# Kernel tuning notes

Measured on AMD Instinct MI355X. Metric: run time of the kernel, lower is better.

## Reference

```python
import jax, jax.numpy as jnp
import numpy as np

C = 1.0
SQRT_C = 1.0
EPS = 1e-6

N_NODES = 50000
N_EDGES = 800000
IN_F = 128   # in_features (weight columns); x has IN_F+1 coords
OUT_F = 128  # out_features; output has OUT_F coords


def l_inner(x, y):
    # Lorentz inner product: -x0*y0 + sum_i xi*yi
    return jnp.sum(x[..., 1:] * y[..., 1:], axis=-1) - x[..., 0] * y[..., 0]


def arcosh(z):
    z = jnp.maximum(z, 1.0 + 1e-7)
    return jnp.log(z + jnp.sqrt(z * z - 1.0))


def log_map_zero(y):
    # log map at origin o=(sqrt(c),0,...,0); result is tangent with head 0
    dist = SQRT_C * arcosh(y[..., 0] / SQRT_C)                      # [N]
    tail = y[..., 1:]
    tail_norm = jnp.sqrt(jnp.maximum(jnp.sum(tail * tail, -1), EPS))
    scaled = (dist / tail_norm)[..., None] * tail
    return jnp.concatenate([jnp.zeros_like(y[..., :1]), scaled], -1)


def exp_map_zero(v):
    # v is a tangent vector at the origin with head component 0
    tail = v[..., 1:]
    n = jnp.sqrt(jnp.maximum(jnp.sum(tail * tail, -1, keepdims=True), EPS))
    n_cut = jnp.minimum(n, 50.0)
    new_tail = SQRT_C * jnp.sinh(n_cut / SQRT_C) * tail / n
    # project onto the hyperboloid: x0 = sqrt(c + ||tail||^2)
    head = jnp.sqrt(C + jnp.sum(new_tail * new_tail, -1, keepdims=True))
    return jnp.concatenate([head, new_tail], -1)


def matvec_regular(weight, x, bias):
    # LGCNLinear forward (eval mode: dropout is identity)
    x_tan = log_map_zero(x)                      # [N, IN_F+1], head = 0
    mx = x_tan[..., 1:] @ weight.T + bias        # [N, OUT_F-1]
    v = jnp.concatenate([x_tan[..., :1], mx], -1)  # head stays 0 (tangent-zero normalized)
    return exp_map_zero(v)                       # [N, OUT_F]


def lorentz_centroid(x, row, col, val):
    # sparse spmm aggregation + Lorentz centroid renormalization
    n = x.shape[0]
    msgs = val[:, None] * x[col]                               # [E, OUT_F] gather
    s = jax.ops.segment_sum(msgs, row, num_segments=n)         # [N, OUT_F] scatter-add
    inner = l_inner(s, s)                                      # [N]
    coef = SQRT_C / jnp.sqrt(jnp.maximum(jnp.abs(inner), EPS))
    return coef[:, None] * s


def hyp_act(x):
    # HypAct: log-map, relu in tangent space, exp-map (c_in == c_out)
    xt = jax.nn.relu(log_map_zero(x))  # head 0 -> relu keeps it 0
    return exp_map_zero(xt)


def setup_inputs() -> dict:
    key = jax.random.key(0)
    k1, k2, k3, k4, k5, k6 = jax.random.split(key, 6)
    tail = 0.5 * jax.random.normal(k1, (N_NODES, IN_F), dtype=jnp.float32)
    head = jnp.sqrt(C + jnp.sum(tail * tail, -1, keepdims=True))
    x = jnp.concatenate([head, tail], -1)                       # on-hyperboloid points
    weight = jax.random.normal(k2, (OUT_F - 1, IN_F), dtype=jnp.float32) * (1.0 / np.sqrt(IN_F))
    bias = 0.01 * jax.random.normal(k3, (OUT_F - 1,), dtype=jnp.float32)
    adj_val = jax.random.uniform(k4, (N_EDGES,), dtype=jnp.float32) / 16.0
    adj_row = jnp.sort(jax.random.randint(k5, (N_EDGES,), 0, N_NODES, dtype=jnp.int32))
    adj_col = jax.random.randint(k6, (N_EDGES,), 0, N_NODES, dtype=jnp.int32)
    return {"x": x, "weight": weight, "bias": bias, "adj_val": adj_val,
            "adj_row": adj_row, "adj_col": adj_col}


def reference(x, weight, bias, adj_val, adj_row, adj_col):
    h = matvec_regular(weight, x, bias)          # hyperbolic linear
    h = lorentz_centroid(h, adj_row, adj_col, adj_val)  # sparse agg + centroid
    h = hyp_act(h)                               # hyperbolic activation
    return h
```

## Files before the change

kernel.cpp:

```cpp
#include <hip/hip_runtime.h>
#include <hip/hip_bf16.h>

#define NN 50000
#define NE 800000

typedef __attribute__((ext_vector_type(4))) float f32x4;
typedef __attribute__((ext_vector_type(8))) __bf16 bf16x8;

__device__ __forceinline__ float wred64(float v) {
    v += __shfl_xor(v, 32, 64);
    v += __shfl_xor(v, 16, 64);
    v += __shfl_xor(v, 8, 64);
    v += __shfl_xor(v, 4, 64);
    v += __shfl_xor(v, 2, 64);
    v += __shfl_xor(v, 1, 64);
    return v;
}

__device__ __forceinline__ float arcosh_f(float z) {
    z = fmaxf(z, 1.0f + 1e-7f);
    return logf(z + sqrtf(z * z - 1.0f));
}

__global__ void prep_rowptr_kernel(const float* __restrict__ weight,
                                   const float* __restrict__ bias,
                                   ushort* __restrict__ WfHi, ushort* __restrict__ WfLo,
                                   float* __restrict__ biasP,
                                   const int* __restrict__ row, int* __restrict__ rowptr) {
    const int b = blockIdx.x;
    if (b < 3125) {
        int e = b * 256 + threadIdx.x;
        if (e >= NE) return;
        int r1 = row[e];
        int r0 = (e == 0) ? -1 : row[e - 1];
        for (int r = r0 + 1; r <= r1; ++r) rowptr[r] = e;
        if (e == NE - 1) {
            for (int r = r1 + 1; r <= NN; ++r) rowptr[r] = NE;
        }
    } else {
        int t8 = (b - 3125) * 256 + threadIdx.x;
        int l = t8 & 63, f = t8 >> 6;
        int t = f & 3, jt = f >> 2;
        int g = l >> 4, r = l & 15;
        int col = jt * 16 + r;
        #pragma unroll
        for (int i = 0; i < 8; ++i) {
            int k = 32 * g + 8 * t + i;
            float v = (col < 127) ? weight[col * 128 + k] : 0.0f;
            __bf16 h = (__bf16)v;
            float lo = v - (float)h;
            __bf16 lb = (__bf16)lo;
            WfHi[t8 * 8 + i] = __builtin_bit_cast(unsigned short, h);
            WfLo[t8 * 8 + i] = __builtin_bit_cast(unsigned short, lb);
        }
        if (t8 < 128) biasP[t8] = (t8 < 127) ? bias[t8] : 0.0f;
    }
}

__global__ __launch_bounds__(256) void transform_kernel(
        const float* __restrict__ x, const ushort* __restrict__ Wf ,
        const float* __restrict__ biasP, ushort* __restrict__ hhb,
        float* __restrict__ hhead) {
    __shared__ __align__(16) ushort WF[32768];

    const int tid = threadIdx.x;
    #pragma unroll
    for (int i = 0; i < 16; ++i)
        ((float4*)WF)[i * 256 + tid] = ((const float4*)Wf)[i * 256 + tid];

    const int lane = tid & 63, w = tid >> 6;
    const int g = lane >> 4, r = lane & 15;
    const int nodeA = blockIdx.x * 64 + w * 16 + r;

    float xv[32];
    float x0 = 1.0f;
    if (nodeA < NN) {
        const float* xp = x + (long)nodeA * 129;
        x0 = xp[0];
        __builtin_memcpy(xv, xp + 1 + 32 * g, 128);
    } else {
        #pragma unroll
        for (int i = 0; i < 32; ++i) xv[i] = 0.0f;
    }
    float dist = arcosh_f(x0);
    float sc = dist / sqrtf(fmaxf(x0 * x0 - 1.0f, 1e-6f));

    bf16x8 ah[4], al[4];
    #pragma unroll
    for (int t = 0; t < 4; ++t) {
        #pragma unroll
        for (int i = 0; i < 8; ++i) {
            float v = sc * xv[8 * t + i];
            __bf16 h = (__bf16)v;
            ah[t][i] = h;
            al[t][i] = (__bf16)(v - (float)h);
        }
    }
    __syncthreads();

    f32x4 acc[8];
    #pragma unroll
    for (int jt = 0; jt < 8; ++jt) acc[jt] = (f32x4){0.0f, 0.0f, 0.0f, 0.0f};

    #pragma unroll
    for (int jt = 0; jt < 8; ++jt) {
        #pragma unroll
        for (int t = 0; t < 4; ++t) {
            const int f = jt * 4 + t;
            bf16x8 bh = *(const bf16x8*)&WF[(f * 64 + lane) * 8];
            bf16x8 bl = *(const bf16x8*)&WF[16384 + (f * 64 + lane) * 8];
            acc[jt] = __builtin_amdgcn_mfma_f32_16x16x32_bf16(al[t], bh, acc[jt], 0, 0, 0);
            acc[jt] = __builtin_amdgcn_mfma_f32_16x16x32_bf16(ah[t], bl, acc[jt], 0, 0, 0);
            acc[jt] = __builtin_amdgcn_mfma_f32_16x16x32_bf16(ah[t], bh, acc[jt], 0, 0, 0);
        }
    }

    float bv[8];
    #pragma unroll
    for (int jt = 0; jt < 8; ++jt) bv[jt] = biasP[jt * 16 + r];

    #pragma unroll
    for (int i = 0; i < 4; ++i) {
        float m[8];
        float p = 0.0f;
        #pragma unroll
        for (int jt = 0; jt < 8; ++jt) {
            m[jt] = acc[jt][i] + bv[jt];
            p = fmaf(m[jt], m[jt], p);
        }
        p += __shfl_xor(p, 1, 64);
        p += __shfl_xor(p, 2, 64);
        p += __shfl_xor(p, 4, 64);
        p += __shfl_xor(p, 8, 64);
        float n = sqrtf(fmaxf(p, 1e-6f));
        float rr = sinhf(fminf(n, 50.0f)) / n;
        int node = blockIdx.x * 64 + w * 16 + g * 4 + i;
        if (node < NN) {
            #pragma unroll
            for (int jt = 0; jt < 8; ++jt) {
                int j = jt * 16 + r;
                float vv = rr * m[jt];
                ushort us = (j == 127) ? (ushort)0
                          : __builtin_bit_cast(unsigned short, (__bf16)vv);
                hhb[node * 128 + j] = us;
            }
            if (r == 15) hhead[node] = sqrtf(1.0f + rr * rr * p);
        }
    }
}

__global__ __launch_bounds__(256) void centroid_act_kernel(
        const ushort* __restrict__ hhb, const float* __restrict__ hhead,
        const float* __restrict__ val, const int* __restrict__ col,
        const int* __restrict__ rowptr, float* __restrict__ out) {
    const int lane = threadIdx.x & 63;
    const int node = __builtin_amdgcn_readfirstlane(blockIdx.x * 4 + (threadIdx.x >> 6));
    const int lo = rowptr[node], hi = rowptr[node + 1];

    float s0p = 0.0f;
    for (int eh = lo + lane; eh < hi; eh += 64) {
        s0p = fmaf(val[eh], hhead[col[eh]], s0p);
    }
    float s0 = wred64(s0p);

    const uint voff = 2u * (uint)lane;
    float sf0 = 0.0f, sf1 = 0.0f;
    for (int e = lo; e < hi; e += 8) {
        const int m = hi - e;
        int c[8]; float v[8];
        #pragma unroll
        for (int k = 0; k < 8; ++k) {
            const int ik = (k < m) ? k : (m - 1);
            c[k] = col[e + ik];
            v[k] = (k < m) ? val[e + ik] : 0.0f;
        }
        uint u[8];
        #pragma unroll
        for (int k = 0; k < 8; ++k)
            u[k] = *(const uint*)&hhb[(((uint)c[k]) << 7) + voff];
        #pragma unroll
        for (int k = 0; k < 8; ++k) {
            sf0 = fmaf(v[k], __builtin_bit_cast(float, u[k] << 16), sf0);
            sf1 = fmaf(v[k], __builtin_bit_cast(float, u[k] & 0xffff0000u), sf1);
        }
    }

    float tsum = wred64(sf0 * sf0 + sf1 * sf1);
    float inner = tsum - s0 * s0;
    float coef = 1.0f / sqrtf(fmaxf(fabsf(inner), 1e-6f));
    float h20 = coef * s0;

    float dist = arcosh_f(h20);
    float tsq = coef * coef * tsum;
    float scl = dist / sqrtf(fmaxf(tsq, 1e-6f));
    float u0 = fmaxf(scl * coef * sf0, 0.0f);
    float u1 = fmaxf(scl * coef * sf1, 0.0f);
    float S = wred64(u0 * u0 + u1 * u1);
    float n = sqrtf(fmaxf(S, 1e-6f));
    float r = sinhf(fminf(n, 50.0f)) / n;

    float* op = out + (long)node * 128;
    op[1 + 2 * lane] = r * u0;
    if (lane < 63) op[2 + 2 * lane] = r * u1;
    else           op[0] = sqrtf(1.0f + r * r * S);
}

extern "C" void kernel_launch(void* const* d_in, const int* in_sizes, int n_in,
                              void* d_out, int out_size, void* d_ws, size_t ws_size,
                              hipStream_t stream) {
    const float* x       = (const float*)d_in[0];
    const float* weight  = (const float*)d_in[1];
    const float* bias    = (const float*)d_in[2];
    const float* adj_val = (const float*)d_in[3];
    const int*   adj_row = (const int*)d_in[4];
    const int*   adj_col = (const int*)d_in[5];
    float* out = (float*)d_out;

    char* ws = (char*)d_ws;
    ushort* hhb    = (ushort*)ws;
    float*  hhead  = (float*)(ws + 12800000);
    int*    rowptr = (int*)(ws + 13000000);
    ushort* WfHi   = (ushort*)(ws + 13200192);
    ushort* WfLo   = (ushort*)(ws + 13232960);
    float*  biasP  = (float*)(ws + 13265728);

    prep_rowptr_kernel<<<3133, 256, 0, stream>>>(weight, bias, WfHi, WfLo, biasP,
                                                 adj_row, rowptr);
    transform_kernel<<<(NN + 63) / 64, 256, 0, stream>>>(x, WfHi, biasP, hhb, hhead);
    centroid_act_kernel<<<NN / 4, 256, 0, stream>>>(hhb, hhead, adj_val, adj_col, rowptr, out);
}
```

Before: 69.81 us.

## Split wavefront into half-waves gathering 8-byte rows and fuse head sum

The centroid kernel now has each half-wave gather a different edge's bf16 row using 8-byte loads, so each lane accumulates four features over half the edges. A cross-half shuffle combines the partial sums. The separate head-coordinate pass over the edge list is folded into the main loop, with eight lanes each handling one edge and the reduced result scaled by 1/8 to undo the replication across the wave. This cuts the number of gather instructions and removes a second walk over col/val, at the cost of more shuffles and only half the lanes writing output.

```diff
diff --git a/kernel.cpp b/kernel.cpp
--- a/kernel.cpp
+++ b/kernel.cpp
@@ -156,17 +156,20 @@
     const int lane = threadIdx.x & 63;
     const int node = __builtin_amdgcn_readfirstlane(blockIdx.x * 4 + (threadIdx.x >> 6));
     const int lo = rowptr[node], hi = rowptr[node + 1];
+    const int h = lane >> 5, q = lane & 31;
+    const int ls = lane & 7;
 
     float s0p = 0.0f;
-    for (int eh = lo + lane; eh < hi; eh += 64) {
-        s0p = fmaf(val[eh], hhead[col[eh]], s0p);
-    }
-    float s0 = wred64(s0p);
-
-    const uint voff = 2u * (uint)lane;
-    float sf0 = 0.0f, sf1 = 0.0f;
+    float sf0 = 0.0f, sf1 = 0.0f, sf2 = 0.0f, sf3 = 0.0f;
+
     for (int e = lo; e < hi; e += 8) {
         const int m = hi - e;
+        {
+            const int ih = (ls < m) ? ls : (m - 1);
+            const int cs = col[e + ih];
+            const float vs = (ls < m) ? val[e + ih] : 0.0f;
+            s0p = fmaf(vs, hhead[cs], s0p);
+        }
         int c[8]; float v[8];
         #pragma unroll
         for (int k = 0; k < 8; ++k) {
@@ -174,35 +177,67 @@
             c[k] = col[e + ik];
             v[k] = (k < m) ? val[e + ik] : 0.0f;
         }
-        uint u[8];
-        #pragma unroll
-        for (int k = 0; k < 8; ++k)
-            u[k] = *(const uint*)&hhb[(((uint)c[k]) << 7) + voff];
-        #pragma unroll
-        for (int k = 0; k < 8; ++k) {
-            sf0 = fmaf(v[k], __builtin_bit_cast(float, u[k] << 16), sf0);
-            sf1 = fmaf(v[k], __builtin_bit_cast(float, u[k] & 0xffff0000u), sf1);
-        }
-    }
-
-    float tsum = wred64(sf0 * sf0 + sf1 * sf1);
-    float inner = tsum - s0 * s0;
-    float coef = 1.0f / sqrtf(fmaxf(fabsf(inner), 1e-6f));
-    float h20 = coef * s0;
-
-    float dist = arcosh_f(h20);
-    float tsq = coef * coef * tsum;
-    float scl = dist / sqrtf(fmaxf(tsq, 1e-6f));
-    float u0 = fmaxf(scl * coef * sf0, 0.0f);
-    float u1 = fmaxf(scl * coef * sf1, 0.0f);
-    float S = wred64(u0 * u0 + u1 * u1);
-    float n = sqrtf(fmaxf(S, 1e-6f));
-    float r = sinhf(fminf(n, 50.0f)) / n;
-
-    float* op = out + (long)node * 128;
-    op[1 + 2 * lane] = r * u0;
-    if (lane < 63) op[2 + 2 * lane] = r * u1;
-    else           op[0] = sqrtf(1.0f + r * r * S);
+        uint2 u[4]; float vp[4];
+        #pragma unroll
+        for (int k = 0; k < 4; ++k) {
+            const int   cp = h ? c[2 * k + 1] : c[2 * k];
+            vp[k]          = h ? v[2 * k + 1] : v[2 * k];
+            u[k] = *(const uint2*)((const char*)hhb + ((((uint)cp) << 8) + ((uint)q << 3)));
+        }
+        #pragma unroll
+        for (int k = 0; k < 4; ++k) {
+            sf0 = fmaf(vp[k], __builtin_bit_cast(float, u[k].x << 16), sf0);
+            sf1 = fmaf(vp[k], __builtin_bit_cast(float, u[k].x & 0xffff0000u), sf1);
+            sf2 = fmaf(vp[k], __builtin_bit_cast(float, u[k].y << 16), sf2);
+            sf3 = fmaf(vp[k], __builtin_bit_cast(float, u[k].y & 0xffff0000u), sf3);
+        }
+    }
+
+    sf0 += __shfl_xor(sf0, 32, 64);
+    sf1 += __shfl_xor(sf1, 32, 64);
+    sf2 += __shfl_xor(sf2, 32, 64);
+    sf3 += __shfl_xor(sf3, 32, 64);
+    float s0 = wred64(s0p) * 0.125f;
+
+    float p2 = sf0 * sf0 + sf1 * sf1 + sf2 * sf2 + sf3 * sf3;
+    p2 += __shfl_xor(p2, 1, 64);
+    p2 += __shfl_xor(p2, 2, 64);
+    p2 += __shfl_xor(p2, 4, 64);
+    p2 += __shfl_xor(p2, 8, 64);
+    p2 += __shfl_xor(p2, 16, 64);
+    const float tsum = p2;
+
+    const float inner = tsum - s0 * s0;
+    const float coef = 1.0f / sqrtf(fmaxf(fabsf(inner), 1e-6f));
+    const float h20 = coef * s0;
+
+    const float dist = arcosh_f(h20);
+    const float tsq = coef * coef * tsum;
+    const float scl = dist / sqrtf(fmaxf(tsq, 1e-6f));
+
+    const float u0 = fmaxf(scl * coef * sf0, 0.0f);
+    const float u1 = fmaxf(scl * coef * sf1, 0.0f);
+    const float u2 = fmaxf(scl * coef * sf2, 0.0f);
+    const float u3 = fmaxf(scl * coef * sf3, 0.0f);
+
+    float p3 = u0 * u0 + u1 * u1 + u2 * u2 + u3 * u3;
+    p3 += __shfl_xor(p3, 1, 64);
+    p3 += __shfl_xor(p3, 2, 64);
+    p3 += __shfl_xor(p3, 4, 64);
+    p3 += __shfl_xor(p3, 8, 64);
+    p3 += __shfl_xor(p3, 16, 64);
+    const float S = p3;
+    const float n = sqrtf(fmaxf(S, 1e-6f));
+    const float r = sinhf(fminf(n, 50.0f)) / n;
+
+    if (h == 0) {
+        float* op = out + (long)node * 128;
+        op[1 + 4 * q] = r * u0;
+        op[2 + 4 * q] = r * u1;
+        op[3 + 4 * q] = r * u2;
+        if (q < 31) op[4 + 4 * q] = r * u3;
+        else        op[0] = sqrtf(1.0f + r * r * S);
+    }
 }
 
 extern "C" void kernel_launch(void* const* d_in, const int* in_sizes, int n_in,
```

After: 140.9 us. 102% more time.
